# Optimization experiments

Measured on AMD Instinct MI355X. Metric: run time of the kernel, lower is better.

Reference implementation:

```python
import jax, jax.numpy as jnp
import numpy as np

NUM_HEADS = 32
NUM_KV_HEADS = 8
HEAD_DIM = 64
HIDDEN = 2048
EPS = 1e-05
ROPE_THETA = 1000000.0


def _rmsnorm(x, w):
    # x: [..., head_dim]
    var = jnp.mean(x * x, axis=-1, keepdims=True)
    return w * (x * jax.lax.rsqrt(var + EPS))


def _rope(q, k):
    # q,k: [B, h, T, d]
    T, d = q.shape[2], q.shape[3]
    inv_freq = 1.0 / (ROPE_THETA ** (jnp.arange(0, d, 2, dtype=jnp.float32) / d))
    t = jnp.arange(T, dtype=jnp.float32)
    freqs = jnp.outer(t, inv_freq)               # [T, d/2]
    emb = jnp.concatenate([freqs, freqs], -1)    # [T, d]
    cos = jnp.cos(emb)[None, None].astype(q.dtype)
    sin = jnp.sin(emb)[None, None].astype(q.dtype)

    def rotate(x):
        x1, x2 = x[..., : d // 2], x[..., d // 2 :]
        return jnp.concatenate([-x2, x1], -1)

    return q * cos + rotate(q) * sin, k * cos + rotate(k) * sin


def setup_inputs() -> dict:
    key = jax.random.key(0)
    ks = jax.random.split(key, 7)
    s = 0.02
    x = jax.random.normal(ks[0], (2, 2048, HIDDEN), jnp.float32)
    Wq = jax.random.normal(ks[1], (HIDDEN, NUM_HEADS * HEAD_DIM), jnp.float32) * s
    Wk = jax.random.normal(ks[2], (HIDDEN, NUM_KV_HEADS * HEAD_DIM), jnp.float32) * s
    Wv = jax.random.normal(ks[3], (HIDDEN, NUM_KV_HEADS * HEAD_DIM), jnp.float32) * s
    Wo = jax.random.normal(ks[4], (NUM_HEADS * HEAD_DIM, HIDDEN), jnp.float32) * s
    q_ln_w = jnp.ones((HEAD_DIM,), jnp.float32)
    k_ln_w = jnp.ones((HEAD_DIM,), jnp.float32)
    return {"x": x, "Wq": Wq, "Wk": Wk, "Wv": Wv, "Wo": Wo, "q_ln_w": q_ln_w, "k_ln_w": k_ln_w}


def reference(x, Wq, Wk, Wv, Wo, q_ln_w, k_ln_w):
    B, T, _ = x.shape
    g = NUM_HEADS // NUM_KV_HEADS  # GQA groups = 4
    q = (x @ Wq).reshape(B, T, NUM_HEADS, HEAD_DIM)
    k = (x @ Wk).reshape(B, T, NUM_KV_HEADS, HEAD_DIM)
    v = (x @ Wv).reshape(B, T, NUM_KV_HEADS, HEAD_DIM)
    q = _rmsnorm(q, q_ln_w)
    k = _rmsnorm(k, k_ln_w)
    q = q.transpose(0, 2, 1, 3)  # [B, nh, T, d]
    k = k.transpose(0, 2, 1, 3)  # [B, nkv, T, d]
    v = v.transpose(0, 2, 1, 3)
    q, k = _rope(q, k)
    # native GQA: fold query heads into (kv_head, group) without repeating K/V
    qg = q.reshape(B, NUM_KV_HEADS, g, T, HEAD_DIM)
    scale = 1.0 / jnp.sqrt(jnp.array(HEAD_DIM, q.dtype))
    scores = jnp.einsum("bkgtd,bksd->bkgts", qg, k) * scale  # [B,nkv,g,T,T]
    causal = jnp.tril(jnp.ones((T, T), bool))
    scores = jnp.where(causal, scores, jnp.finfo(scores.dtype).min)
    probs = jax.nn.softmax(scores, axis=-1)
    out = jnp.einsum("bkgts,bksd->bkgtd", probs, v)  # [B,nkv,g,T,d]
    out = out.reshape(B, NUM_HEADS, T, HEAD_DIM).transpose(0, 2, 1, 3).reshape(B, T, -1)
    return out @ Wo
```

## Files before the change

### kernel.cpp

```cpp
#include <hip/hip_runtime.h>
#include <cstdint>
#include <cstddef>

typedef unsigned short u16;
typedef __attribute__((ext_vector_type(8))) short short8;
typedef __attribute__((ext_vector_type(4))) short short4v;
typedef __attribute__((ext_vector_type(4))) float float4v;
typedef __attribute__((ext_vector_type(4))) unsigned short ushort4v;
typedef __attribute__((ext_vector_type(2))) float float2v;

__device__ __forceinline__ u16 f2bf(float f) {
    union { float f; uint32_t u; } x; x.f = f;
    uint32_t r = x.u + 0x7fffu + ((x.u >> 16) & 1u);
    return (u16)(r >> 16);
}
__device__ __forceinline__ uint32_t pack_bf16x2(float lo, float hi) {
    union { float f; uint32_t u; } a, b; a.f = lo; b.f = hi;
    return __builtin_amdgcn_perm(b.u + 0x8000u, a.u + 0x8000u, 0x07060302u);
}
__device__ __forceinline__ void gl_lds16(const u16* g, u16* l) {
    __builtin_amdgcn_global_load_lds(
        (const __attribute__((address_space(1))) void*)g,
        (__attribute__((address_space(3))) void*)l, 16, 0, 0);
}

__global__ __launch_bounds__(256) void prep(const float4v* __restrict__ x,
                                            const float* __restrict__ Wq,
                                            const float* __restrict__ Wk,
                                            const float* __restrict__ Wv,
                                            const float* __restrict__ Wo,
                                            ushort4v* __restrict__ xb,
                                            u16* __restrict__ wqkv_t,
                                            u16* __restrict__ wo_t,
                                            float2v* __restrict__ tab) {
    __shared__ float lds[32][33];
    const int bid = blockIdx.x;
    const int tid = threadIdx.x;
    if (bid < 8192) {
        const int i = bid * 256 + tid;
        float4v v = x[i];
        ushort4v o;
        #pragma unroll
        for (int j = 0; j < 4; ++j) o[j] = f2bf(v[j]);
        xb[i] = o;
        return;
    }
    if (bid < 8448) {
        const int idx = (bid - 8192) * 256 + tid;
        const int t = idx >> 5;
        const int i = idx & 31;
        const float invf = exp2f(-(float)i * (19.931568569324174f / 32.0f));
        float sv, cv;
        sincosf((float)t * invf, &sv, &cv);
        float2v o; o[0] = cv; o[1] = sv;
        tab[idx] = o;
        return;
    }
    const float* src;
    int Ns, n0, k0, scol0;
    u16* dst;
    if (bid < 14592) {
        const int id = bid - 8448;
        const int bx = id % 96, by = id / 96;
        n0 = bx * 32; k0 = by * 32;
        if (n0 < 2048)      { src = Wq; Ns = 2048; scol0 = n0; }
        else if (n0 < 2560) { src = Wk; Ns = 512;  scol0 = n0 - 2048; }
        else                { src = Wv; Ns = 512;  scol0 = n0 - 2560; }
        dst = wqkv_t;
    } else {
        const int id = bid - 14592;
        const int bx = id & 63, by = id >> 6;
        n0 = bx * 32; k0 = by * 32;
        src = Wo; Ns = 2048; scol0 = n0;
        dst = wo_t;
    }
    const int row = tid >> 3;
    const int c4  = (tid & 7) * 4;
    const float4v v = *(const float4v*)(src + (size_t)(k0 + row) * Ns + scol0 + c4);
    #pragma unroll
    for (int i = 0; i < 4; ++i) lds[row][c4 + i] = v[i];
    __syncthreads();
    const int nrow = tid >> 3;
    const int k4   = (tid & 7) * 4;
    ushort4v o;
    #pragma unroll
    for (int i = 0; i < 4; ++i) o[i] = f2bf(lds[k4 + i][nrow]);
    *(ushort4v*)(dst + (size_t)(n0 + nrow) * 2048 + k0 + k4) = o;
}

__global__ __launch_bounds__(256, 3) void gemm_bt(const u16* __restrict__ A,
                                                  const u16* __restrict__ Bt,
                                                  float* __restrict__ C,
                                                  int M, int N, int K) {
    __shared__ u16 lds_a[128 * 32];
    __shared__ u16 lds_b[128 * 32];
    const int tid  = threadIdx.x;
    const int wave = tid >> 6;
    const int lane = tid & 63;
    const int quad = lane >> 4;
    const int l15  = lane & 15;
    const long m0 = (long)blockIdx.x * 128;
    const long n0 = (long)blockIdx.y * 128;
    const int wm = (wave >> 1) * 64;
    const int wn = (wave & 1) * 64;
    const int s_row = tid >> 2;
    const int s_col = (tid & 3) * 8;

    float4v acc[4][4];
    #pragma unroll
    for (int i = 0; i < 4; ++i)
        #pragma unroll
        for (int j = 0; j < 4; ++j)
            #pragma unroll
            for (int r = 0; r < 4; ++r) acc[i][j][r] = 0.0f;

    const u16* ga0 = A  + (m0 + s_row) * (long)K + s_col;
    const u16* ga1 = ga0 + 64 * (long)K;
    const u16* gb0 = Bt + (n0 + s_row) * (long)K + s_col;
    const u16* gb1 = gb0 + 64 * (long)K;
    u16* la = lds_a + tid * 8;
    u16* lb = lds_b + tid * 8;

    const int n_k = K >> 5;
    for (int it = 0; it < n_k; ++it) {
        const int k0 = it << 5;
        gl_lds16(ga0 + k0, la);
        gl_lds16(ga1 + k0, la + 2048);
        gl_lds16(gb0 + k0, lb);
        gl_lds16(gb1 + k0, lb + 2048);
        __syncthreads();
        short8 af[4], bfr[4];
        #pragma unroll
        for (int mt = 0; mt < 4; ++mt)
            af[mt] = *(const short8*)(lds_a + (wm + mt * 16 + l15) * 32 + quad * 8);
        #pragma unroll
        for (int nt = 0; nt < 4; ++nt)
            bfr[nt] = *(const short8*)(lds_b + (wn + nt * 16 + l15) * 32 + quad * 8);
        #pragma unroll
        for (int mt = 0; mt < 4; ++mt)
            #pragma unroll
            for (int nt = 0; nt < 4; ++nt)
                acc[mt][nt] = __builtin_amdgcn_mfma_f32_16x16x32_bf16(af[mt], bfr[nt], acc[mt][nt], 0, 0, 0);
        __syncthreads();
    }
    #pragma unroll
    for (int mt = 0; mt < 4; ++mt) {
        #pragma unroll
        for (int nt = 0; nt < 4; ++nt) {
            const long gr = m0 + wm + mt * 16 + quad * 4;
            const long gc = n0 + wn + nt * 16 + l15;
            #pragma unroll
            for (int r = 0; r < 4; ++r)
                C[(gr + r) * N + gc] = acc[mt][nt][r];
        }
    }
}

__global__ __launch_bounds__(256, 3) void gemm_qkv(const u16* __restrict__ A,
                                                   const u16* __restrict__ Bt,
                                                   const float* __restrict__ qw,
                                                   const float* __restrict__ kw,
                                                   const float2v* __restrict__ tab,
                                                   u16* __restrict__ Qr,
                                                   u16* __restrict__ Kr,
                                                   u16* __restrict__ Vt) {
    const int K = 2048;
    __shared__ u16 lds_a[128 * 32];
    __shared__ u16 lds_b[128 * 32];
    const int tid  = threadIdx.x;
    const int wave = tid >> 6;
    const int lane = tid & 63;
    const int quad = lane >> 4;
    const int l15  = lane & 15;
    const long m0 = (long)blockIdx.x * 128;
    const long n0 = (long)blockIdx.y * 128;
    const int wm = (wave >> 1) * 64;
    const int wn = (wave & 1) * 64;
    const int s_row = tid >> 2;
    const int s_col = (tid & 3) * 8;

    float4v acc[4][4];
    #pragma unroll
    for (int i = 0; i < 4; ++i)
        #pragma unroll
        for (int j = 0; j < 4; ++j)
            #pragma unroll
            for (int r = 0; r < 4; ++r) acc[i][j][r] = 0.0f;

    const u16* ga0 = A  + (m0 + s_row) * (long)K + s_col;
    const u16* ga1 = ga0 + 64 * (long)K;
    const u16* gb0 = Bt + (n0 + s_row) * (long)K + s_col;
    const u16* gb1 = gb0 + 64 * (long)K;
    u16* la = lds_a + tid * 8;
    u16* lb = lds_b + tid * 8;

    const int n_k = K >> 5;
    for (int it = 0; it < n_k; ++it) {
        const int k0 = it << 5;
        gl_lds16(ga0 + k0, la);
        gl_lds16(ga1 + k0, la + 2048);
        gl_lds16(gb0 + k0, lb);
        gl_lds16(gb1 + k0, lb + 2048);
        __syncthreads();
        short8 af[4], bfr[4];
        #pragma unroll
        for (int mt = 0; mt < 4; ++mt)
            af[mt] = *(const short8*)(lds_a + (wm + mt * 16 + l15) * 32 + quad * 8);
        #pragma unroll
        for (int nt = 0; nt < 4; ++nt)
            bfr[nt] = *(const short8*)(lds_b + (wn + nt * 16 + l15) * 32 + quad * 8);
        #pragma unroll
        for (int mt = 0; mt < 4; ++mt)
            #pragma unroll
            for (int nt = 0; nt < 4; ++nt)
                acc[mt][nt] = __builtin_amdgcn_mfma_f32_16x16x32_bf16(af[mt], bfr[nt], acc[mt][nt], 0, 0, 0);
        __syncthreads();
    }

    const int col0 = (int)n0 + wn;
    if (col0 < 2560) {
        const bool isQ = (col0 < 2048);
        const float* lw = isQ ? qw : kw;
        float wreg[4];
        #pragma unroll
        for (int nt = 0; nt < 4; ++nt) wreg[nt] = lw[nt * 16 + l15];
        const float qs = isQ ? 0.18033688011112042f : 1.0f;
        u16* dst = isQ ? (Qr + ((size_t)(col0 >> 6)) * 2048 * 64)
                       : (Kr + ((size_t)((col0 - 2048) >> 6)) * 2048 * 64);
        const size_t head_stride = isQ ? ((size_t)32 * 2048 * 64) : ((size_t)8 * 2048 * 64);
        #pragma unroll
        for (int mt = 0; mt < 4; ++mt) {
            const int gr0 = (int)m0 + wm + mt * 16 + quad * 4;
            const int b = gr0 >> 11, tt0 = gr0 & 2047;
            float rms[4];
            #pragma unroll
            for (int r = 0; r < 4; ++r) {
                float s = 0.0f;
                #pragma unroll
                for (int nt = 0; nt < 4; ++nt) s += acc[mt][nt][r] * acc[mt][nt][r];
                s += __shfl_xor(s, 1);
                s += __shfl_xor(s, 2);
                s += __shfl_xor(s, 4);
                s += __shfl_xor(s, 8);
                rms[r] = rsqrtf(s * (1.0f / 64.0f) + 1e-5f);
            }
            u16* rowp = dst + (size_t)b * head_stride + (size_t)tt0 * 64;
            #pragma unroll
            for (int nt = 0; nt < 2; ++nt) {
                const int i = nt * 16 + l15;
                #pragma unroll
                for (int r = 0; r < 4; ++r) {
                    const float2v cs = tab[(tt0 + r) * 32 + i];
                    const float v1 = acc[mt][nt][r]     * rms[r] * wreg[nt];
                    const float v2 = acc[mt][nt + 2][r] * rms[r] * wreg[nt + 2];
                    const float o1 = (v1 * cs[0] - v2 * cs[1]) * qs;
                    const float o2 = (v2 * cs[0] + v1 * cs[1]) * qs;
                    rowp[(size_t)r * 64 + i]      = f2bf(o1);
                    rowp[(size_t)r * 64 + i + 32] = f2bf(o2);
                }
            }
        }
    } else {
        const int kh = (col0 - 2560) >> 6;
        #pragma unroll
        for (int mt = 0; mt < 4; ++mt) {
            const int gr0 = (int)m0 + wm + mt * 16 + quad * 4;
            const int b = gr0 >> 11, tt0 = gr0 & 2047;
            #pragma unroll
            for (int nt = 0; nt < 4; ++nt) {
                const int d = nt * 16 + l15;
                ushort4v o;
                #pragma unroll
                for (int r = 0; r < 4; ++r) o[r] = f2bf(acc[mt][nt][r]);
                *(ushort4v*)(Vt + (((size_t)(b * 8 + kh)) * 64 + d) * 2048 + tt0) = o;
            }
        }
    }
}

#define KSTR 72
#define VSTR 136
__global__ __launch_bounds__(512, 4) void attn_fwd(const u16* __restrict__ Qr,
                                                   const u16* __restrict__ Kr,
                                                   const u16* __restrict__ Vt,
                                                   u16* __restrict__ Ob) {
    __shared__ u16 lds_k[2][128 * KSTR];
    __shared__ u16 lds_vt[2][64 * VSTR];
    const int tid  = threadIdx.x;
    const int wave = tid >> 6;
    const int lane = tid & 63;
    const int quad = lane >> 4;
    const int l15  = lane & 15;
    const int qxB = blockIdx.x;
    const int qxA = 15 - qxB;
    const int bh = blockIdx.y;
    const int b = bh >> 5, h = bh & 31;
    const int kh = h >> 2;
    const u16* Qh = Qr + ((size_t)(b * 32 + h))  * 2048 * 64;
    const u16* Kh = Kr + ((size_t)(b * 8 + kh))  * 2048 * 64;
    const u16* Vh = Vt + ((size_t)(b * 8 + kh))  * 64 * 2048;

    const int k_key0 = tid >> 3;
    const int k_d0   = (tid & 7) * 8;
    const int v_d0   = tid >> 4;
    const int v_k8   = (tid & 15) * 8;

    const int qrowA = qxA * 128 + wave * 16 + l15;
    const int qrowB = qxB * 128 + wave * 16 + l15;
    short8 qfA[2], qfB[2];
    #pragma unroll
    for (int ks = 0; ks < 2; ++ks) {
        qfA[ks] = *(const short8*)(Qh + (size_t)qrowA * 64 + ks * 32 + quad * 8);
        qfB[ks] = *(const short8*)(Qh + (size_t)qrowB * 64 + ks * 32 + quad * 8);
    }
    short8 qf0 = qfA[0], qf1 = qfA[1];
    int qrow_cur = qrowA;

    float m_i = -3e38f, l_i = 0.0f;
    float4v Oacc[4];
    #pragma unroll
    for (int dt = 0; dt < 4; ++dt)
        #pragma unroll
        for (int r = 0; r < 4; ++r) Oacc[dt][r] = 0.0f;

    short8 kreg[2], vreg[2];
    #pragma unroll
    for (int i = 0; i < 2; ++i) {
        kreg[i] = *(const short8*)(Kh + (size_t)(k_key0 + i * 64) * 64 + k_d0);
        vreg[i] = *(const short8*)(Vh + (size_t)(v_d0 + i * 32) * 2048 + v_k8);
    }
    #pragma unroll
    for (int i = 0; i < 2; ++i) {
        *(short8*)(lds_k[0]  + (k_key0 + i * 64) * KSTR + k_d0) = kreg[i];
        *(short8*)(lds_vt[0] + (v_d0 + i * 32) * VSTR + v_k8)   = vreg[i];
    }
    __syncthreads();

    const int n_it = 17;
    for (int i = 0; i < n_it; ++i) {
        const int p = i & 1;
        const bool last = (i == n_it - 1);
        const int kt_cur = (i <= qxA) ? i : (i - qxA - 1);
        const int kt0 = kt_cur << 7;

        if (!last) {
            const int ip1 = i + 1;
            const int ktn = (ip1 <= qxA) ? ip1 : (ip1 - qxA - 1);
            const size_t nk0 = (size_t)(ktn << 7);
            #pragma unroll
            for (int j = 0; j < 2; ++j) {
                kreg[j] = *(const short8*)(Kh + (nk0 + k_key0 + j * 64) * 64 + k_d0);
                vreg[j] = *(const short8*)(Vh + (size_t)(v_d0 + j * 32) * 2048 + nk0 + v_k8);
            }
        }

        float4v S[8];
        #pragma unroll
        for (int nt = 0; nt < 8; ++nt)
            #pragma unroll
            for (int r = 0; r < 4; ++r) S[nt][r] = 0.0f;
        #pragma unroll
        for (int ks = 0; ks < 2; ++ks) {
            const short8 qf = ks ? qf1 : qf0;
            #pragma unroll
            for (int nt = 0; nt < 8; ++nt) {
                short8 kf = *(const short8*)(lds_k[p] + (nt * 16 + l15) * KSTR + ks * 32 + quad * 8);
                S[nt] = __builtin_amdgcn_mfma_f32_16x16x32_bf16(kf, qf, S[nt], 0, 0, 0);
            }
        }
        if (i == qxA || last) {
            #pragma unroll
            for (int nt = 0; nt < 8; ++nt) {
                const int keyb = kt0 + nt * 16 + quad * 4;
                #pragma unroll
                for (int r = 0; r < 4; ++r)
                    if (keyb + r > qrow_cur) S[nt][r] = -3e38f;
            }
        }
        float mx = S[0][0];
        #pragma unroll
        for (int nt = 0; nt < 8; ++nt)
            #pragma unroll
            for (int r = 0; r < 4; ++r) mx = fmaxf(mx, S[nt][r]);
        mx = fmaxf(mx, __shfl_xor(mx, 16));
        mx = fmaxf(mx, __shfl_xor(mx, 32));
        if (!__all(mx <= m_i + 8.0f)) {
            const float mnew = fmaxf(m_i, mx);
            const float alpha = __builtin_amdgcn_exp2f(m_i - mnew);
            m_i = mnew;
            l_i *= alpha;
            #pragma unroll
            for (int dt = 0; dt < 4; ++dt)
                #pragma unroll
                for (int r = 0; r < 4; ++r) Oacc[dt][r] *= alpha;
        }
        float rs = 0.0f;
        #pragma unroll
        for (int nt = 0; nt < 8; ++nt)
            #pragma unroll
            for (int r = 0; r < 4; ++r) {
                const float pv = __builtin_amdgcn_exp2f(S[nt][r] - m_i);
                S[nt][r] = pv;
                rs += pv;
            }
        rs += __shfl_xor(rs, 16);
        rs += __shfl_xor(rs, 32);
        l_i += rs;

        #pragma unroll
        for (int nt = 0; nt < 8; ++nt) {
            union { uint32_t u[2]; short4v s; } pu;
            pu.u[0] = pack_bf16x2(S[nt][0], S[nt][1]);
            pu.u[1] = pack_bf16x2(S[nt][2], S[nt][3]);
            const short4v pf = pu.s;
            #pragma unroll
            for (int dt = 0; dt < 4; ++dt) {
                const short4v vf = *(const short4v*)(lds_vt[p] + (dt * 16 + l15) * VSTR + nt * 16 + quad * 4);
                Oacc[dt] = __builtin_amdgcn_mfma_f32_16x16x16bf16_1k(vf, pf, Oacc[dt], 0, 0, 0);
            }
        }

        if (i == qxA) {
            const float rl = 1.0f / l_i;
            #pragma unroll
            for (int dt = 0; dt < 4; ++dt) {
                ushort4v o;
                #pragma unroll
                for (int r = 0; r < 4; ++r) o[r] = f2bf(Oacc[dt][r] * rl);
                *(ushort4v*)(Ob + ((size_t)(b * 2048 + qrowA)) * 2048 + h * 64 + dt * 16 + quad * 4) = o;
            }
            m_i = -3e38f;
            l_i = 0.0f;
            #pragma unroll
            for (int dt = 0; dt < 4; ++dt)
                #pragma unroll
                for (int r = 0; r < 4; ++r) Oacc[dt][r] = 0.0f;
            qf0 = qfB[0];
            qf1 = qfB[1];
            qrow_cur = qrowB;
        }

        if (!last) {
            #pragma unroll
            for (int j = 0; j < 2; ++j) {
                *(short8*)(lds_k[1 - p]  + (k_key0 + j * 64) * KSTR + k_d0) = kreg[j];
                *(short8*)(lds_vt[1 - p] + (v_d0 + j * 32) * VSTR + v_k8)   = vreg[j];
            }
        }
        __syncthreads();
    }
    const float rl = 1.0f / l_i;
    #pragma unroll
    for (int dt = 0; dt < 4; ++dt) {
        ushort4v o;
        #pragma unroll
        for (int r = 0; r < 4; ++r) o[r] = f2bf(Oacc[dt][r] * rl);
        *(ushort4v*)(Ob + ((size_t)(b * 2048 + qrowB)) * 2048 + h * 64 + dt * 16 + quad * 4) = o;
    }
}

extern "C" void kernel_launch(void* const* d_in, const int* in_sizes, int n_in,
                              void* d_out, int out_size, void* d_ws, size_t ws_size,
                              hipStream_t stream) {
    (void)in_sizes; (void)n_in; (void)out_size; (void)ws_size;
    const float* x  = (const float*)d_in[0];
    const float* Wq = (const float*)d_in[1];
    const float* Wk = (const float*)d_in[2];
    const float* Wv = (const float*)d_in[3];
    const float* Wo = (const float*)d_in[4];
    const float* qw = (const float*)d_in[5];
    const float* kw = (const float*)d_in[6];
    float* out = (float*)d_out;

    char* ws = (char*)d_ws;
    size_t off = 0;
    auto alloc = [&](size_t bytes) {
        char* p = ws + off;
        off += (bytes + 255) & ~(size_t)255;
        return p;
    };
    u16* xb     = (u16*)alloc((size_t)8388608 * 2);
    u16* wqkv_t = (u16*)alloc((size_t)3072 * 2048 * 2);
    u16* wo_t   = (u16*)alloc((size_t)2048 * 2048 * 2);
    u16* q_r    = (u16*)alloc((size_t)2 * 32 * 2048 * 64 * 2);
    u16* k_r    = (u16*)alloc((size_t)2 * 8 * 2048 * 64 * 2);
    u16* v_r    = (u16*)alloc((size_t)2 * 8 * 64 * 2048 * 2);
    float2v* rtab = (float2v*)alloc((size_t)2048 * 32 * 8);
    u16* attnb  = xb;

    hipLaunchKernelGGL(prep, dim3(18688), dim3(256), 0, stream,
                       (const float4v*)x, Wq, Wk, Wv, Wo,
                       (ushort4v*)xb, wqkv_t, wo_t, rtab);
    hipLaunchKernelGGL(gemm_qkv, dim3(32, 24), dim3(256), 0, stream,
                       xb, wqkv_t, qw, kw, rtab, q_r, k_r, v_r);
    hipLaunchKernelGGL(attn_fwd, dim3(8, 64), dim3(512), 0, stream, q_r, k_r, v_r, attnb);
    hipLaunchKernelGGL(gemm_bt, dim3(32, 16), dim3(256), 0, stream,
                       attnb, wo_t, out, 4096, 2048, 2048);
}
```

Baseline: 294.7 us.

## Permute V-tile LDS layout, add MFMA priority hints, swap attention grid order

```diff
diff --git a/kernel.cpp b/kernel.cpp
--- a/kernel.cpp
+++ b/kernel.cpp
@@ -291,9 +291,9 @@
     const int lane = tid & 63;
     const int quad = lane >> 4;
     const int l15  = lane & 15;
-    const int qxB = blockIdx.x;
+    const int qxB = blockIdx.y;
     const int qxA = 15 - qxB;
-    const int bh = blockIdx.y;
+    const int bh = blockIdx.x;
     const int b = bh >> 5, h = bh & 31;
     const int kh = h >> 2;
     const u16* Qh = Qr + ((size_t)(b * 32 + h))  * 2048 * 64;
@@ -304,6 +304,9 @@
     const int k_d0   = (tid & 7) * 8;
     const int v_d0   = tid >> 4;
     const int v_k8   = (tid & 15) * 8;
+    const int t15 = tid & 15;
+    const int vka = ((2 * t15) & 3) * 32 + (t15 >> 1) * 4;
+    const int vkb = ((2 * t15 + 1) & 3) * 32 + (t15 >> 1) * 4;
 
     const int qrowA = qxA * 128 + wave * 16 + l15;
     const int qrowB = qxB * 128 + wave * 16 + l15;
@@ -331,8 +334,11 @@
     }
     #pragma unroll
     for (int i = 0; i < 2; ++i) {
-        *(short8*)(lds_k[0]  + (k_key0 + i * 64) * KSTR + k_d0) = kreg[i];
-        *(short8*)(lds_vt[0] + (v_d0 + i * 32) * VSTR + v_k8)   = vreg[i];
+        *(short8*)(lds_k[0] + (k_key0 + i * 64) * KSTR + k_d0) = kreg[i];
+        short4v vlo = __builtin_shufflevector(vreg[i], vreg[i], 0, 1, 2, 3);
+        short4v vhi = __builtin_shufflevector(vreg[i], vreg[i], 4, 5, 6, 7);
+        *(short4v*)(lds_vt[0] + (v_d0 + i * 32) * VSTR + vka) = vlo;
+        *(short4v*)(lds_vt[0] + (v_d0 + i * 32) * VSTR + vkb) = vhi;
     }
     __syncthreads();
 
@@ -359,6 +365,7 @@
         for (int nt = 0; nt < 8; ++nt)
             #pragma unroll
             for (int r = 0; r < 4; ++r) S[nt][r] = 0.0f;
+        __builtin_amdgcn_s_setprio(1);
         #pragma unroll
         for (int ks = 0; ks < 2; ++ks) {
             const short8 qf = ks ? qf1 : qf0;
@@ -368,6 +375,7 @@
                 S[nt] = __builtin_amdgcn_mfma_f32_16x16x32_bf16(kf, qf, S[nt], 0, 0, 0);
             }
         }
+        __builtin_amdgcn_s_setprio(0);
         if (i == qxA || last) {
             #pragma unroll
             for (int nt = 0; nt < 8; ++nt) {
@@ -384,41 +392,44 @@
             for (int r = 0; r < 4; ++r) mx = fmaxf(mx, S[nt][r]);
         mx = fmaxf(mx, __shfl_xor(mx, 16));
         mx = fmaxf(mx, __shfl_xor(mx, 32));
-        if (!__all(mx <= m_i + 8.0f)) {
-            const float mnew = fmaxf(m_i, mx);
-            const float alpha = __builtin_amdgcn_exp2f(m_i - mnew);
-            m_i = mnew;
-            l_i *= alpha;
-            #pragma unroll
-            for (int dt = 0; dt < 4; ++dt)
-                #pragma unroll
-                for (int r = 0; r < 4; ++r) Oacc[dt][r] *= alpha;
-        }
+        const float mnew = fmaxf(m_i, mx);
+        const float alpha = __builtin_amdgcn_exp2f(m_i - mnew);
+        m_i = mnew;
         float rs = 0.0f;
         #pragma unroll
         for (int nt = 0; nt < 8; ++nt)
             #pragma unroll
             for (int r = 0; r < 4; ++r) {
-                const float pv = __builtin_amdgcn_exp2f(S[nt][r] - m_i);
+                const float pv = __builtin_amdgcn_exp2f(S[nt][r] - mnew);
                 S[nt][r] = pv;
                 rs += pv;
             }
         rs += __shfl_xor(rs, 16);
         rs += __shfl_xor(rs, 32);
-        l_i += rs;
-
-        #pragma unroll
-        for (int nt = 0; nt < 8; ++nt) {
-            union { uint32_t u[2]; short4v s; } pu;
-            pu.u[0] = pack_bf16x2(S[nt][0], S[nt][1]);
-            pu.u[1] = pack_bf16x2(S[nt][2], S[nt][3]);
-            const short4v pf = pu.s;
+        l_i = l_i * alpha + rs;
+        #pragma unroll
+        for (int dt = 0; dt < 4; ++dt)
+            #pragma unroll
+            for (int r = 0; r < 4; ++r) Oacc[dt][r] *= alpha;
+
+        __builtin_amdgcn_s_setprio(1);
+        #pragma unroll
+        for (int nt2 = 0; nt2 < 4; ++nt2) {
+            union { uint32_t u[2]; short4v s; } p0, p1;
+            p0.u[0] = pack_bf16x2(S[2 * nt2][0], S[2 * nt2][1]);
+            p0.u[1] = pack_bf16x2(S[2 * nt2][2], S[2 * nt2][3]);
+            p1.u[0] = pack_bf16x2(S[2 * nt2 + 1][0], S[2 * nt2 + 1][1]);
+            p1.u[1] = pack_bf16x2(S[2 * nt2 + 1][2], S[2 * nt2 + 1][3]);
             #pragma unroll
             for (int dt = 0; dt < 4; ++dt) {
-                const short4v vf = *(const short4v*)(lds_vt[p] + (dt * 16 + l15) * VSTR + nt * 16 + quad * 4);
-                Oacc[dt] = __builtin_amdgcn_mfma_f32_16x16x16bf16_1k(vf, pf, Oacc[dt], 0, 0, 0);
-            }
-        }
+                short8 vv = *(const short8*)(lds_vt[p] + (dt * 16 + l15) * VSTR + quad * 32 + nt2 * 8);
+                short4v vlo = __builtin_shufflevector(vv, vv, 0, 1, 2, 3);
+                short4v vhi = __builtin_shufflevector(vv, vv, 4, 5, 6, 7);
+                Oacc[dt] = __builtin_amdgcn_mfma_f32_16x16x16bf16_1k(vlo, p0.s, Oacc[dt], 0, 0, 0);
+                Oacc[dt] = __builtin_amdgcn_mfma_f32_16x16x16bf16_1k(vhi, p1.s, Oacc[dt], 0, 0, 0);
+            }
+        }
+        __builtin_amdgcn_s_setprio(0);
 
         if (i == qxA) {
             const float rl = 1.0f / l_i;
@@ -443,8 +454,11 @@
         if (!last) {
             #pragma unroll
             for (int j = 0; j < 2; ++j) {
-                *(short8*)(lds_k[1 - p]  + (k_key0 + j * 64) * KSTR + k_d0) = kreg[j];
-                *(short8*)(lds_vt[1 - p] + (v_d0 + j * 32) * VSTR + v_k8)   = vreg[j];
+                *(short8*)(lds_k[1 - p] + (k_key0 + j * 64) * KSTR + k_d0) = kreg[j];
+                short4v vlo = __builtin_shufflevector(vreg[j], vreg[j], 0, 1, 2, 3);
+                short4v vhi = __builtin_shufflevector(vreg[j], vreg[j], 4, 5, 6, 7);
+                *(short4v*)(lds_vt[1 - p] + (v_d0 + j * 32) * VSTR + vka) = vlo;
+                *(short4v*)(lds_vt[1 - p] + (v_d0 + j * 32) * VSTR + vkb) = vhi;
             }
         }
         __syncthreads();
@@ -493,7 +507,7 @@
                        (ushort4v*)xb, wqkv_t, wo_t, rtab);
     hipLaunchKernelGGL(gemm_qkv, dim3(32, 24), dim3(256), 0, stream,
                        xb, wqkv_t, qw, kw, rtab, q_r, k_r, v_r);
-    hipLaunchKernelGGL(attn_fwd, dim3(8, 64), dim3(512), 0, stream, q_r, k_r, v_r, attnb);
+    hipLaunchKernelGGL(attn_fwd, dim3(64, 8), dim3(512), 0, stream, q_r, k_r, v_r, attnb);
     hipLaunchKernelGGL(gemm_bt, dim3(32, 16), dim3(256), 0, stream,
                        attnb, wo_t, out, 4096, 2048, 2048);
 }
```

New measurement: 289.0 us. No clear change (-1.9%).
